# Performance work log

Measured on AMD Instinct MI355X. Metric: run time of the kernel, lower is better.

The kernel has to match this reference:

```python
import jax, jax.numpy as jnp
import numpy as np

N_SAMPLES = 4194304
N_RAYS = 65536


def setup_inputs() -> dict:
    key = jax.random.key(0)
    k1, k2, k3 = jax.random.split(key, 3)
    rgb_samples = jax.random.uniform(k1, (N_SAMPLES, 3), dtype=jnp.float32)
    weights_samples = jax.random.uniform(k2, (N_SAMPLES, 1), dtype=jnp.float32)
    ray_indices = jnp.sort(jax.random.randint(k3, (N_SAMPLES,), 0, N_RAYS, dtype=jnp.int32))
    return {
        "rgb_samples": rgb_samples,
        "weights_samples": weights_samples,
        "ray_indices": ray_indices,
        "n_rays": N_RAYS,
    }


def reference(rgb_samples, weights_samples, ray_indices, n_rays):
    # Packed/ragged per-ray weighted color integration:
    # pred_rgb[r] = sum_{i in ray r} weights[i] * rgb[i]
    weighted = rgb_samples * weights_samples  # [N_samples, 3]
    pred_rgb = jax.ops.segment_sum(weighted, ray_indices, num_segments=n_rays)  # [N_rays, 3]
    return pred_rgb
```

## Files before the change

### kernel.cpp

```cpp
#include <hip/hip_runtime.h>


#define V 8

__global__ __launch_bounds__(256) void integrate_kernel(
    const float* __restrict__ rgb,
    const float* __restrict__ w,
    const int*   __restrict__ idx,
    float*       __restrict__ out,
    int n)
{
    const int lane = threadIdx.x & 63;
    const long long wave = ((long long)blockIdx.x * blockDim.x + threadIdx.x) >> 6;
    const long long base = wave * (64LL * V);
    if (base >= n) return;

    int   ids[V];
    float vx[V], vy[V], vz[V];
    #pragma unroll
    for (int u = 0; u < V; ++u) {
        long long s  = base + (long long)u * 64 + lane;
        bool      ok = (s < n);
        long long sc = ok ? s : (n - 1);
        int   id = idx[sc];
        float wv = ok ? w[sc] : 0.0f;
        float r  = rgb[3 * sc + 0];
        float g  = rgb[3 * sc + 1];
        float b  = rgb[3 * sc + 2];
        ids[u] = id;
        vx[u] = wv * r;
        vy[u] = wv * g;
        vz[u] = wv * b;
    }

    #pragma unroll
    for (int u = 0; u < V; ++u) {
        int   id = ids[u];
        float ax = vx[u], ay = vy[u], az = vz[u];

        int  prev = __shfl_up(id, 1);
        bool head = (lane == 0) || (prev != id);
        unsigned long long hm = __ballot(head);

        #pragma unroll
        for (int d = 1; d < 64; d <<= 1) {
            float ox = __shfl_down(ax, d);
            float oy = __shfl_down(ay, d);
            float oz = __shfl_down(az, d);
            unsigned long long between =
                (hm >> (lane + 1)) & ((1ull << d) - 1ull);
            bool cont = (lane + d < 64) && (between == 0);
            if (cont) { ax += ox; ay += oy; az += oz; }
        }

        if (head) {
            atomicAdd(&out[id * 3 + 0], ax);
            atomicAdd(&out[id * 3 + 1], ay);
            atomicAdd(&out[id * 3 + 2], az);
        }
    }
}

extern "C" void kernel_launch(void* const* d_in, const int* in_sizes, int n_in,
                              void* d_out, int out_size, void* d_ws, size_t ws_size,
                              hipStream_t stream) {
    const float* rgb = (const float*)d_in[0];
    const float* w   = (const float*)d_in[1];
    const int*   idx = (const int*)  d_in[2];
    float*       out = (float*)d_out;

    int n = in_sizes[2];

    hipMemsetAsync(d_out, 0, (size_t)out_size * sizeof(float), stream);

    long long waves  = ((long long)n + 64LL * V - 1) / (64LL * V);
    long long blocks = (waves + 3) / 4;
    integrate_kernel<<<(int)blocks, 256, 0, stream>>>(rgb, w, idx, out, n);
}
```

Before: 110.6 us.

## Give each lane contiguous samples with vector loads and one wave-level segmented scan

After: 111.3 us. No clear change (+0.6%).

```diff
diff --git a/kernel.cpp b/kernel.cpp
--- a/kernel.cpp
+++ b/kernel.cpp
@@ -1,9 +1,10 @@
 #include <hip/hip_runtime.h>
 
 
-#define V 8
+#define SPL 8
+#define WAVE_SAMPLES (64 * SPL)
 
-__global__ __launch_bounds__(256) void integrate_kernel(
+__global__ __launch_bounds__(256, 6) void integrate_kernel(
     const float* __restrict__ rgb,
     const float* __restrict__ w,
     const int*   __restrict__ idx,
@@ -11,53 +12,94 @@
     int n)
 {
     const int lane = threadIdx.x & 63;
-    const long long wave = ((long long)blockIdx.x * blockDim.x + threadIdx.x) >> 6;
-    const long long base = wave * (64LL * V);
-    if (base >= n) return;
+    const long long wave  = ((long long)blockIdx.x * blockDim.x + threadIdx.x) >> 6;
+    const long long wbase = wave * WAVE_SAMPLES;
+    if (wbase >= n) return;
+    const long long base = wbase + (long long)lane * SPL;
 
-    int   ids[V];
-    float vx[V], vy[V], vz[V];
-    #pragma unroll
-    for (int u = 0; u < V; ++u) {
-        long long s  = base + (long long)u * 64 + lane;
-        bool      ok = (s < n);
-        long long sc = ok ? s : (n - 1);
-        int   id = idx[sc];
-        float wv = ok ? w[sc] : 0.0f;
-        float r  = rgb[3 * sc + 0];
-        float g  = rgb[3 * sc + 1];
-        float b  = rgb[3 * sc + 2];
-        ids[u] = id;
-        vx[u] = wv * r;
-        vy[u] = wv * g;
-        vz[u] = wv * b;
+    int   ids[SPL];
+    float ws[SPL], sx[SPL], sy[SPL], sz[SPL];
+
+    if (base + SPL <= n) {
+        int4   i0 = *(const int4*)(idx + base);
+        int4   i1 = *(const int4*)(idx + base + 4);
+        float4 w0 = *(const float4*)(w + base);
+        float4 w1 = *(const float4*)(w + base + 4);
+        const float4* r4 = (const float4*)(rgb + 3 * base);
+        float4 r0 = r4[0], r1 = r4[1], r2 = r4[2];
+        float4 r3 = r4[3], r4v = r4[4], r5 = r4[5];
+
+        ids[0]=i0.x; ids[1]=i0.y; ids[2]=i0.z; ids[3]=i0.w;
+        ids[4]=i1.x; ids[5]=i1.y; ids[6]=i1.z; ids[7]=i1.w;
+        ws[0]=w0.x; ws[1]=w0.y; ws[2]=w0.z; ws[3]=w0.w;
+        ws[4]=w1.x; ws[5]=w1.y; ws[6]=w1.z; ws[7]=w1.w;
+        sx[0]=r0.x;  sy[0]=r0.y;  sz[0]=r0.z;
+        sx[1]=r0.w;  sy[1]=r1.x;  sz[1]=r1.y;
+        sx[2]=r1.z;  sy[2]=r1.w;  sz[2]=r2.x;
+        sx[3]=r2.y;  sy[3]=r2.z;  sz[3]=r2.w;
+        sx[4]=r3.x;  sy[4]=r3.y;  sz[4]=r3.z;
+        sx[5]=r3.w;  sy[5]=r4v.x; sz[5]=r4v.y;
+        sx[6]=r4v.z; sy[6]=r4v.w; sz[6]=r5.x;
+        sx[7]=r5.y;  sy[7]=r5.z;  sz[7]=r5.w;
+    } else {
+        #pragma unroll
+        for (int k = 0; k < SPL; ++k) {
+            long long s  = base + k;
+            bool      ok = (s < n);
+            long long sc = ok ? s : (long long)(n - 1);
+            ids[k] = idx[sc];
+            ws[k]  = ok ? w[sc] : 0.0f;
+            sx[k] = rgb[3*sc+0]; sy[k] = rgb[3*sc+1]; sz[k] = rgb[3*sc+2];
+        }
     }
 
+    const int first = ids[0];
+    int   cur = first;
+    float ax = ws[0]*sx[0], ay = ws[0]*sy[0], az = ws[0]*sz[0];
+    float hx = 0.f, hy = 0.f, hz = 0.f;
+    bool  f = false;
     #pragma unroll
-    for (int u = 0; u < V; ++u) {
-        int   id = ids[u];
-        float ax = vx[u], ay = vy[u], az = vz[u];
+    for (int k = 1; k < SPL; ++k) {
+        if (ids[k] != cur) {
+            if (!f) { hx = ax; hy = ay; hz = az; f = true; }
+            else {
+                atomicAdd(&out[cur*3+0], ax);
+                atomicAdd(&out[cur*3+1], ay);
+                atomicAdd(&out[cur*3+2], az);
+            }
+            ax = ay = az = 0.f;
+            cur = ids[k];
+        }
+        ax = fmaf(ws[k], sx[k], ax);
+        ay = fmaf(ws[k], sy[k], ay);
+        az = fmaf(ws[k], sz[k], az);
+    }
+    const int t_id = cur;
 
-        int  prev = __shfl_up(id, 1);
-        bool head = (lane == 0) || (prev != id);
-        unsigned long long hm = __ballot(head);
+    int  t_prev = __shfl_up(t_id, 1);
+    bool brk    = f || (lane > 0 && t_prev != first);
+    unsigned long long bm = __ballot(brk);
 
-        #pragma unroll
-        for (int d = 1; d < 64; d <<= 1) {
-            float ox = __shfl_down(ax, d);
-            float oy = __shfl_down(ay, d);
-            float oz = __shfl_down(az, d);
-            unsigned long long between =
-                (hm >> (lane + 1)) & ((1ull << d) - 1ull);
-            bool cont = (lane + d < 64) && (between == 0);
-            if (cont) { ax += ox; ay += oy; az += oz; }
-        }
+    float Sx = ax, Sy = ay, Sz = az;
+    #pragma unroll
+    for (int d = 1; d < 64; d <<= 1) {
+        float ox = __shfl_down(Sx, d);
+        float oy = __shfl_down(Sy, d);
+        float oz = __shfl_down(Sz, d);
+        unsigned long long between = ((bm >> 1) >> lane) & ((1ull << d) - 1ull);
+        bool cont = (lane + d < 64) && (between == 0);
+        if (cont) { Sx += ox; Sy += oy; Sz += oz; }
+    }
 
-        if (head) {
-            atomicAdd(&out[id * 3 + 0], ax);
-            atomicAdd(&out[id * 3 + 1], ay);
-            atomicAdd(&out[id * 3 + 2], az);
-        }
+    if (lane == 0 || brk) {
+        atomicAdd(&out[t_id*3+0], Sx);
+        atomicAdd(&out[t_id*3+1], Sy);
+        atomicAdd(&out[t_id*3+2], Sz);
+    }
+    if (f) {
+        atomicAdd(&out[first*3+0], hx);
+        atomicAdd(&out[first*3+1], hy);
+        atomicAdd(&out[first*3+2], hz);
     }
 }
 
@@ -73,7 +115,7 @@
 
     hipMemsetAsync(d_out, 0, (size_t)out_size * sizeof(float), stream);
 
-    long long waves  = ((long long)n + 64LL * V - 1) / (64LL * V);
+    long long waves  = ((long long)n + WAVE_SAMPLES - 1) / WAVE_SAMPLES;
     long long blocks = (waves + 3) / 4;
     integrate_kernel<<<(int)blocks, 256, 0, stream>>>(rgb, w, idx, out, n);
 }
```

## Replace atomic segmented scan with CSR ray offsets and per-ray wave reduction

Applied to the files above, without the earlier changes.

Measured after the change: 115.8 us. 4.7% more time.

```diff
diff --git a/kernel.cpp b/kernel.cpp
--- a/kernel.cpp
+++ b/kernel.cpp
@@ -1,63 +1,74 @@
 #include <hip/hip_runtime.h>
 
 
-#define V 8
+#define A_SPT 8
 
-__global__ __launch_bounds__(256) void integrate_kernel(
+__global__ __launch_bounds__(256) void ray_start_kernel(
+    const int* __restrict__ idx,
+    int*       __restrict__ ray_start,
+    int n, int n_rays)
+{
+    long long base = ((long long)blockIdx.x * blockDim.x + threadIdx.x) * A_SPT;
+    if (base >= n) return;
+
+    int v[A_SPT + 1];
+    if (base + A_SPT < n) {
+        int4 a = *(const int4*)(idx + base);
+        int4 b = *(const int4*)(idx + base + 4);
+        v[0]=a.x; v[1]=a.y; v[2]=a.z; v[3]=a.w;
+        v[4]=b.x; v[5]=b.y; v[6]=b.z; v[7]=b.w;
+        v[8] = idx[base + 8];
+    } else {
+        #pragma unroll
+        for (int k = 0; k <= A_SPT; ++k) {
+            long long s = base + k;
+            v[k] = (s < n) ? idx[s] : n_rays;
+        }
+    }
+
+    if (base == 0) {
+        for (int q = 0; q <= v[0]; ++q) ray_start[q] = 0;
+    }
+    #pragma unroll
+    for (int k = 0; k < A_SPT; ++k) {
+        int a = v[k], b = v[k + 1];
+        for (int q = a + 1; q <= b; ++q) ray_start[q] = (int)(base + k + 1);
+    }
+}
+
+__global__ __launch_bounds__(256) void integrate_rays_kernel(
     const float* __restrict__ rgb,
     const float* __restrict__ w,
-    const int*   __restrict__ idx,
+    const int*   __restrict__ ray_start,
     float*       __restrict__ out,
-    int n)
+    int n_rays)
 {
     const int lane = threadIdx.x & 63;
-    const long long wave = ((long long)blockIdx.x * blockDim.x + threadIdx.x) >> 6;
-    const long long base = wave * (64LL * V);
-    if (base >= n) return;
+    const int ray  = blockIdx.x * (blockDim.x >> 6) + (threadIdx.x >> 6);
+    if (ray >= n_rays) return;
 
-    int   ids[V];
-    float vx[V], vy[V], vz[V];
-    #pragma unroll
-    for (int u = 0; u < V; ++u) {
-        long long s  = base + (long long)u * 64 + lane;
-        bool      ok = (s < n);
-        long long sc = ok ? s : (n - 1);
-        int   id = idx[sc];
-        float wv = ok ? w[sc] : 0.0f;
-        float r  = rgb[3 * sc + 0];
-        float g  = rgb[3 * sc + 1];
-        float b  = rgb[3 * sc + 2];
-        ids[u] = id;
-        vx[u] = wv * r;
-        vy[u] = wv * g;
-        vz[u] = wv * b;
+    const int s0 = ray_start[ray];
+    const int s1 = ray_start[ray + 1];
+
+    float ax = 0.f, ay = 0.f, az = 0.f;
+    for (int s = s0 + lane; s < s1; s += 64) {
+        float wv = w[s];
+        ax = fmaf(wv, rgb[3 * s + 0], ax);
+        ay = fmaf(wv, rgb[3 * s + 1], ay);
+        az = fmaf(wv, rgb[3 * s + 2], az);
     }
 
     #pragma unroll
-    for (int u = 0; u < V; ++u) {
-        int   id = ids[u];
-        float ax = vx[u], ay = vy[u], az = vz[u];
+    for (int d = 1; d < 64; d <<= 1) {
+        ax += __shfl_down(ax, d);
+        ay += __shfl_down(ay, d);
+        az += __shfl_down(az, d);
+    }
 
-        int  prev = __shfl_up(id, 1);
-        bool head = (lane == 0) || (prev != id);
-        unsigned long long hm = __ballot(head);
-
-        #pragma unroll
-        for (int d = 1; d < 64; d <<= 1) {
-            float ox = __shfl_down(ax, d);
-            float oy = __shfl_down(ay, d);
-            float oz = __shfl_down(az, d);
-            unsigned long long between =
-                (hm >> (lane + 1)) & ((1ull << d) - 1ull);
-            bool cont = (lane + d < 64) && (between == 0);
-            if (cont) { ax += ox; ay += oy; az += oz; }
-        }
-
-        if (head) {
-            atomicAdd(&out[id * 3 + 0], ax);
-            atomicAdd(&out[id * 3 + 1], ay);
-            atomicAdd(&out[id * 3 + 2], az);
-        }
+    if (lane == 0) {
+        out[3 * ray + 0] = ax;
+        out[3 * ray + 1] = ay;
+        out[3 * ray + 2] = az;
     }
 }
 
@@ -68,12 +79,16 @@
     const float* w   = (const float*)d_in[1];
     const int*   idx = (const int*)  d_in[2];
     float*       out = (float*)d_out;
+    int*   ray_start = (int*)d_ws;
 
-    int n = in_sizes[2];
+    int n      = in_sizes[2];
+    int n_rays = out_size / 3;
 
-    hipMemsetAsync(d_out, 0, (size_t)out_size * sizeof(float), stream);
+    long long a_threads = ((long long)n + A_SPT - 1) / A_SPT;
+    int a_blocks = (int)((a_threads + 255) / 256);
+    ray_start_kernel<<<a_blocks, 256, 0, stream>>>(idx, ray_start, n, n_rays);
 
-    long long waves  = ((long long)n + 64LL * V - 1) / (64LL * V);
-    long long blocks = (waves + 3) / 4;
-    integrate_kernel<<<(int)blocks, 256, 0, stream>>>(rgb, w, idx, out, n);
+    int rays_per_block = 256 / 64;
+    int b_blocks = (n_rays + rays_per_block - 1) / rays_per_block;
+    integrate_rays_kernel<<<b_blocks, 256, 0, stream>>>(rgb, w, ray_start, out, n_rays);
 }
```
